# Kernel tuning notes

Measured on AMD Instinct MI355X. Metric: run time of the kernel, lower is better.

## Reference

```python
import jax, jax.numpy as jnp
import numpy as np
from jax import lax

B, W, RSS, NLED, LED_F, HID = 8192, 512, 12, 16, 8, 64


def setup_inputs() -> dict:
    key = jax.random.key(0)
    ks = jax.random.split(key, 20)
    s = 0.05
    return {
        "rss_chunk": jax.random.normal(ks[0], (B, W, RSS), jnp.float32),
        "anchor_pos": jax.random.normal(ks[1], (B, 3), jnp.float32),
        "led_feats": jax.random.normal(ks[2], (NLED, LED_F), jnp.float32),
        "led_positions": jax.random.normal(ks[3], (NLED, 3), jnp.float32),
        "freq_mask": jax.random.randint(ks[4], (RSS, NLED), 0, 2, jnp.int32),
        # temporal_conv params (torch Conv1d weight layout [out, in, k])
        "conv1_w": jax.random.normal(ks[5], (32, RSS, 3), jnp.float32) * s,
        "conv1_b": jax.random.normal(ks[6], (32,), jnp.float32) * s,
        "conv2_w": jax.random.normal(ks[7], (64, 32, 3), jnp.float32) * s,
        "conv2_b": jax.random.normal(ks[8], (64,), jnp.float32) * s,
        # projections (torch Linear weight layout [out, in])
        "q_w": jax.random.normal(ks[9], (64, W + 3), jnp.float32) * s,
        "q_b": jax.random.normal(ks[10], (64,), jnp.float32) * s,
        "k_w": jax.random.normal(ks[11], (64, LED_F + 3), jnp.float32) * s,
        "k_b": jax.random.normal(ks[12], (64,), jnp.float32) * s,
        "red_w": jax.random.normal(ks[13], (64, RSS * LED_F), jnp.float32) * s,
        "red_b": jax.random.normal(ks[14], (64,), jnp.float32) * s,
        "fus_w": jax.random.normal(ks[15], (HID, 64 + 64), jnp.float32) * s,
        "fus_b": jax.random.normal(ks[16], (HID,), jnp.float32) * s,
    }


def _conv1d(x, w, b, stride):
    # x: [B, C_in, L], w: [C_out, C_in, k], padding 1
    y = lax.conv_general_dilated(x, w, (stride,), [(1, 1)],
                                 dimension_numbers=("NCH", "OIH", "NCH"))
    return y + b[None, :, None]


def reference(rss_chunk, anchor_pos, led_feats, led_positions, freq_mask,
              conv1_w, conv1_b, conv2_w, conv2_b,
              q_w, q_b, k_w, k_b, red_w, red_b, fus_w, fus_b):
    Bc = rss_chunk.shape[0]
    x = jnp.swapaxes(rss_chunk, 1, 2)                       # [B, 12, W]

    # temporal conv branch -> [B, 64]
    h = jax.nn.relu(_conv1d(x, conv1_w, conv1_b, 1))        # [B, 32, W]
    h = jax.nn.relu(_conv1d(h, conv2_w, conv2_b, 2))        # [B, 64, W//2]
    t_feat = h.mean(axis=-1)                                # AdaptiveAvgPool1d(1)

    # queries: [B, 12, W+3] -> [B, 12, 64]
    pos_rep = jnp.broadcast_to(anchor_pos[:, None, :], (Bc, RSS, 3))
    query_in = jnp.concatenate([x, pos_rep], axis=-1)
    queries = query_in @ q_w.T + q_b

    # keys: [N, 11] -> [N, 64] (shared across batch)
    key_in = jnp.concatenate([led_feats, led_positions], axis=-1)
    keys = key_in @ k_w.T + k_b

    scores = jnp.einsum("brd,nd->brn", queries, keys)       # [B, 12, N]
    dist_sq = jnp.sum((anchor_pos[:, None, :] - led_positions[None, :, :]) ** 2, -1)
    dist_bias = 0.5 * jnp.log(1.0 / (dist_sq + 1e-8))       # [B, N]
    scores = scores + dist_bias[:, None, :]
    scores = jnp.where(freq_mask[None] == 0, jnp.finfo(scores.dtype).min, scores)

    attn = jax.nn.softmax(scores, axis=-1)                  # [B, 12, N]
    s_agg = jnp.einsum("brn,nf->brf", attn, led_feats)      # [B, 12, 8]
    s_feat = jax.nn.relu(s_agg.reshape(Bc, -1) @ red_w.T + red_b)  # [B, 64]

    combined = jnp.concatenate([t_feat, s_feat], axis=-1)   # [B, 128]
    return combined @ fus_w.T + fus_b                       # [B, hidden]
```

## Files before the change

kernel.cpp:

```cpp
#include <hip/hip_runtime.h>
#include <float.h>
#include <math.h>

typedef __bf16 bf16;
typedef __attribute__((ext_vector_type(8))) __bf16 bf16x8;
typedef __attribute__((ext_vector_type(4))) float f32x4;
typedef long long i64;

#define MK 544

#define WS_MG   0
#define WS_CVEC 17408
#define WS_W1F  17472
#define WS_W2F  19520

__device__ __forceinline__ f32x4 mfma16(bf16x8 a, bf16x8 b, f32x4 c) {
  return __builtin_amdgcn_mfma_f32_16x16x32_bf16(a, b, c, 0, 0, 0);
}
__device__ __forceinline__ f32x4 mfma8(i64 a, i64 b, f32x4 c) {
  return __builtin_amdgcn_mfma_f32_16x16x32_fp8_fp8(a, b, c, 0, 0, 0);
}

__global__ __launch_bounds__(256) void acek_pre(
    const float* __restrict__ led_feats, const float* __restrict__ led_pos,
    const float* __restrict__ q_w, const float* __restrict__ q_b,
    const float* __restrict__ k_w, const float* __restrict__ k_b,
    const float* __restrict__ c1w, const float* __restrict__ c2w,
    char* __restrict__ ws) {
  bf16* Mg = (bf16*)(ws + WS_MG);
  float* cvec = (float*)(ws + WS_CVEC);
  i64* W1F = (i64*)(ws + WS_W1F);
  i64* W2F = (i64*)(ws + WS_W2F);
  const int t = threadIdx.x;

  if (blockIdx.x == 34) {
    {
      int ot = t >> 7, s = (t >> 6) & 1, lane = t & 63;
      int g = lane >> 4, a15 = lane & 15;
      float v[8];
#pragma unroll
      for (int j = 0; j < 8; ++j) {
        int k1 = s * 32 + g * 8 + j;
        int dk = k1 >> 4, ic = k1 & 15;
        v[j] = (ic < 12 && dk < 3) ? 16.f * c1w[(ot * 16 + a15) * 36 + ic * 3 + dk] : 0.f;
      }
      int lo = __builtin_amdgcn_cvt_pk_fp8_f32(v[0], v[1], 0, false);
      lo = __builtin_amdgcn_cvt_pk_fp8_f32(v[2], v[3], lo, true);
      int hi = __builtin_amdgcn_cvt_pk_fp8_f32(v[4], v[5], 0, false);
      hi = __builtin_amdgcn_cvt_pk_fp8_f32(v[6], v[7], hi, true);
      W1F[t] = ((i64)(unsigned)lo) | (((i64)hi) << 32);
    }
    for (int r = 0; r < 3; ++r) {
      int fi = t + r * 256;
      int o = fi / 192, rem = fi - o * 192;
      int s = rem >> 6, lane = rem & 63;
      int g = lane >> 4, a15 = lane & 15;
      float v[8];
#pragma unroll
      for (int j = 0; j < 8; ++j)
        v[j] = 16.f * c2w[(o * 16 + a15) * 96 + (g * 8 + j) * 3 + s];
      int lo = __builtin_amdgcn_cvt_pk_fp8_f32(v[0], v[1], 0, false);
      lo = __builtin_amdgcn_cvt_pk_fp8_f32(v[2], v[3], lo, true);
      int hi = __builtin_amdgcn_cvt_pk_fp8_f32(v[4], v[5], 0, false);
      hi = __builtin_amdgcn_cvt_pk_fp8_f32(v[6], v[7], hi, true);
      W2F[fi] = ((i64)(unsigned)lo) | (((i64)hi) << 32);
    }
    return;
  }

  __shared__ float keys[16 * 64];
  for (int idx = t; idx < 16 * 64; idx += 256) {
    int n = idx >> 6, d = idx & 63;
    float acc = k_b[d];
#pragma unroll
    for (int j = 0; j < 8; ++j) acc += k_w[d * 11 + j] * led_feats[n * 8 + j];
#pragma unroll
    for (int j = 0; j < 3; ++j) acc += k_w[d * 11 + 8 + j] * led_pos[n * 3 + j];
    keys[idx] = acc;
  }
  __syncthreads();
  int e = blockIdx.x * 256 + t;
  if (e < 16 * MK) {
    int n = e / MK, k = e - n * MK;
    float v = 0.f;
    if (k < 515) {
#pragma unroll 4
      for (int d = 0; d < 64; ++d) v += q_w[d * 515 + k] * keys[n * 64 + d];
    }
    Mg[e] = (bf16)v;
  }
  if (blockIdx.x == 0 && t < 16) {
    float acc = 0.f;
    for (int d = 0; d < 64; ++d) acc += q_b[d] * keys[t * 64 + d];
    cvec[t] = acc;
  }
}

__global__ __launch_bounds__(256, 4) void acek_main(
    const float* __restrict__ rss, const float* __restrict__ anchor,
    const float* __restrict__ ledf, const float* __restrict__ ledp,
    const int* __restrict__ fmask,
    const float* __restrict__ c1b, const float* __restrict__ c2b,
    const float* __restrict__ rw, const float* __restrict__ rb,
    const float* __restrict__ fw, const float* __restrict__ fb,
    const bf16* __restrict__ Mg, const float* __restrict__ cvec,
    const i64* __restrict__ W1F, const i64* __restrict__ W2F,
    float* __restrict__ out) {

  __shared__ __align__(16) unsigned char xw8[515 * 16];
  __shared__ __align__(16) unsigned char h1[513 * 32];
  __shared__ __align__(16) float parts[1024];
  __shared__ __align__(16) float sagg[96];
  __shared__ __align__(16) float bias_lds[16];
  float* tfp = (float*)xw8;
  float* comb = (float*)(xw8 + 1024);

  const int tid = threadIdx.x;
  const int lane = tid & 63;
  const int wv = tid >> 6;
  const int a15 = lane & 15;
  const int g = lane >> 4;
  const int b = blockIdx.x;
  char* xwb = (char*)xw8;
  char* h1b = (char*)h1;

  i64 w1f[2][2];
#pragma unroll
  for (int ot = 0; ot < 2; ++ot)
#pragma unroll
    for (int s = 0; s < 2; ++s) w1f[ot][s] = W1F[(ot * 2 + s) * 64 + lane];
  i64 w2f[4][3];
#pragma unroll
  for (int o = 0; o < 4; ++o)
#pragma unroll
    for (int s = 0; s < 3; ++s) w2f[o][s] = W2F[(o * 3 + s) * 64 + lane];
  f32x4 b1v[2], b2s[4];
#pragma unroll
  for (int ot = 0; ot < 2; ++ot) b1v[ot] = *(const f32x4*)&c1b[ot * 16 + g * 4];
#pragma unroll
  for (int o = 0; o < 4; ++o) {
    f32x4 tmp = *(const f32x4*)&c2b[o * 16 + g * 4];
    b2s[o] = tmp * 16.f;
  }

  for (int r = tid; r < 515; r += 256) *(int*)(xwb + r * 16 + 12) = 0;
  if (tid < 12) {
    int rr = (tid >> 2) == 0 ? 0 : ((tid >> 2) == 1 ? 513 : 514);
    *(int*)(xwb + rr * 16 + (tid & 3) * 4) = 0;
  }
  if (tid < 4) *(i64*)(h1b + tid * 8) = 0;
  if (tid < 16) {
    float dx = anchor[(size_t)b * 3 + 0] - ledp[tid * 3 + 0];
    float dy = anchor[(size_t)b * 3 + 1] - ledp[tid * 3 + 1];
    float dz = anchor[(size_t)b * 3 + 2] - ledp[tid * 3 + 2];
    bias_lds[tid] = cvec[tid] - 0.5f * __logf(dx * dx + dy * dy + dz * dz + 1e-8f);
  }

  const float* xb = rss + (size_t)b * 6144;
#pragma unroll
  for (int i = 0; i < 6; ++i) {
    int f = tid + i * 256;
    f32x4 v = ((const f32x4*)xb)[f];
    int w = f / 3;
    int c = (f - w * 3) * 4;
    int pk = __builtin_amdgcn_cvt_pk_fp8_f32(16.f * v[0], 16.f * v[1], 0, false);
    pk = __builtin_amdgcn_cvt_pk_fp8_f32(16.f * v[2], 16.f * v[3], pk, true);
    *(int*)(xwb + (w + 1) * 16 + c) = pk;
  }
  __syncthreads();

  {
    const int rcl = (a15 < 12) ? a15 : 11;
    float sav[4][8];
#pragma unroll
    for (int t = 0; t < 4; ++t) {
      const int s = 4 * t + wv;
      const float* xs = xb + (s * 32 + g * 8) * 12 + rcl;
#pragma unroll
      for (int j = 0; j < 8; ++j) sav[t][j] = xs[j * 12];
    }
    float anc0 = 0.f, anc1 = 0.f, anc2 = 0.f;
    if (wv == 0) {
      anc0 = anchor[(size_t)b * 3 + 0];
      anc1 = anchor[(size_t)b * 3 + 1];
      anc2 = anchor[(size_t)b * 3 + 2];
    }

#pragma unroll
    for (int t = 0; t < 8; ++t) {
      const int wt = wv * 8 + t;
      const int wcol = wt * 16 + a15;
      f32x4 c0 = {0.f, 0.f, 0.f, 0.f}, c1 = {0.f, 0.f, 0.f, 0.f};
#pragma unroll
      for (int s = 0; s < 2; ++s) {
        int row = wcol + 2 * s + (g >> 1);
        i64 bv = *(const i64*)(xwb + row * 16 + ((g & 1) << 3));
        c0 = mfma8(w1f[0][s], bv, c0);
        c1 = mfma8(w1f[1][s], bv, c1);
      }
      const int hrow = wcol + 1;
      const int swz = (hrow >> 2) & 3;
      const int off0 = ((((g >> 1) + 0) ^ swz) << 3) | ((g & 1) << 2);
      const int off1 = ((((g >> 1) + 2) ^ swz) << 3) | ((g & 1) << 2);
      float v0 = fmaxf(fmaf(c0[0], 0.00390625f, b1v[0][0]), 0.f);
      float v1 = fmaxf(fmaf(c0[1], 0.00390625f, b1v[0][1]), 0.f);
      float v2 = fmaxf(fmaf(c0[2], 0.00390625f, b1v[0][2]), 0.f);
      float v3 = fmaxf(fmaf(c0[3], 0.00390625f, b1v[0][3]), 0.f);
      int pk0 = __builtin_amdgcn_cvt_pk_fp8_f32(v0, v1, 0, false);
      pk0 = __builtin_amdgcn_cvt_pk_fp8_f32(v2, v3, pk0, true);
      *(int*)(h1b + hrow * 32 + off0) = pk0;
      v0 = fmaxf(fmaf(c1[0], 0.00390625f, b1v[1][0]), 0.f);
      v1 = fmaxf(fmaf(c1[1], 0.00390625f, b1v[1][1]), 0.f);
      v2 = fmaxf(fmaf(c1[2], 0.00390625f, b1v[1][2]), 0.f);
      v3 = fmaxf(fmaf(c1[3], 0.00390625f, b1v[1][3]), 0.f);
      int pk1 = __builtin_amdgcn_cvt_pk_fp8_f32(v0, v1, 0, false);
      pk1 = __builtin_amdgcn_cvt_pk_fp8_f32(v2, v3, pk1, true);
      *(int*)(h1b + hrow * 32 + off1) = pk1;
    }

    const bf16* MgR = Mg + a15 * MK;
    f32x4 sac = {0.f, 0.f, 0.f, 0.f};
#pragma unroll
    for (int t = 0; t < 4; ++t) {
      const int s = 4 * t + wv;
      bf16x8 av;
#pragma unroll
      for (int j = 0; j < 8; ++j) av[j] = (bf16)sav[t][j];
      bf16x8 bm = *(const bf16x8*)&MgR[s * 32 + g * 8];
      sac = mfma16(av, bm, sac);
    }
    if (wv == 0) {
      bf16x8 av = {(bf16)0.f, (bf16)0.f, (bf16)0.f, (bf16)0.f,
                   (bf16)0.f, (bf16)0.f, (bf16)0.f, (bf16)0.f};
      if (g == 0) { av[0] = (bf16)anc0; av[1] = (bf16)anc1; av[2] = (bf16)anc2; }
      bf16x8 bm = *(const bf16x8*)&MgR[512 + g * 8];
      sac = mfma16(av, bm, sac);
    }
#pragma unroll
    for (int r = 0; r < 4; ++r)
      parts[wv * 256 + (g * 4 + r) * 16 + a15] = sac[r];
  }
  __syncthreads();

  {
    float tacc[4][4] = {{0.f, 0.f, 0.f, 0.f}, {0.f, 0.f, 0.f, 0.f},
                        {0.f, 0.f, 0.f, 0.f}, {0.f, 0.f, 0.f, 0.f}};
#pragma unroll
    for (int pti = 0; pti < 4; ++pti) {
      const int p = (wv * 4 + pti) * 16 + a15;
      f32x4 cc0 = {0.f, 0.f, 0.f, 0.f}, cc1 = {0.f, 0.f, 0.f, 0.f};
      f32x4 cc2 = {0.f, 0.f, 0.f, 0.f}, cc3 = {0.f, 0.f, 0.f, 0.f};
#pragma unroll
      for (int s = 0; s < 3; ++s) {
        const int rho = 2 * p + s;
        i64 hv = *(const i64*)(h1b + rho * 32 + ((g ^ ((rho >> 2) & 3)) << 3));
        cc0 = mfma8(w2f[0][s], hv, cc0);
        cc1 = mfma8(w2f[1][s], hv, cc1);
        cc2 = mfma8(w2f[2][s], hv, cc2);
        cc3 = mfma8(w2f[3][s], hv, cc3);
      }
#pragma unroll
      for (int r = 0; r < 4; ++r) {
        tacc[0][r] += fmaxf(cc0[r] + b2s[0][r], 0.f);
        tacc[1][r] += fmaxf(cc1[r] + b2s[1][r], 0.f);
        tacc[2][r] += fmaxf(cc2[r] + b2s[2][r], 0.f);
        tacc[3][r] += fmaxf(cc3[r] + b2s[3][r], 0.f);
      }
    }
#pragma unroll
    for (int o = 0; o < 4; ++o)
#pragma unroll
      for (int r = 0; r < 4; ++r) {
        float v = tacc[o][r];
        v += __shfl_xor(v, 1, 16);
        v += __shfl_xor(v, 2, 16);
        v += __shfl_xor(v, 4, 16);
        v += __shfl_xor(v, 8, 16);
        if (a15 == 0) tfp[wv * 64 + o * 16 + g * 4 + r] = v;
      }
  }
  __syncthreads();

  if (tid < 192) {
    const int r = tid >> 4, n = tid & 15;
    float s = parts[tid] + parts[256 + tid] + parts[512 + tid] + parts[768 + tid];
    s += bias_lds[n];
    if (fmask[r * 16 + n] == 0) s = -FLT_MAX;
    float mx = s;
    mx = fmaxf(mx, __shfl_xor(mx, 1, 16));
    mx = fmaxf(mx, __shfl_xor(mx, 2, 16));
    mx = fmaxf(mx, __shfl_xor(mx, 4, 16));
    mx = fmaxf(mx, __shfl_xor(mx, 8, 16));
    float ev = __expf(s - mx);
    float sm = ev;
    sm += __shfl_xor(sm, 1, 16);
    sm += __shfl_xor(sm, 2, 16);
    sm += __shfl_xor(sm, 4, 16);
    sm += __shfl_xor(sm, 8, 16);
    const float attv = ev / sm;
#pragma unroll
    for (int f = 0; f < 8; ++f) {
      float c = attv * ledf[n * 8 + f];
      c += __shfl_xor(c, 1, 16);
      c += __shfl_xor(c, 2, 16);
      c += __shfl_xor(c, 4, 16);
      c += __shfl_xor(c, 8, 16);
      if (n == f) sagg[r * 8 + f] = c;
    }
  } else {
    const int t64 = tid - 192;
    comb[t64] = (tfp[t64] + tfp[64 + t64] + tfp[128 + t64] + tfp[192 + t64]) *
                (1.f / 4096.f);
  }
  __syncthreads();

  {
    const int o = tid >> 2, q = tid & 3;
    float acc = 0.f;
    const f32x4* rwv = (const f32x4*)(rw + o * 96 + q * 24);
    const f32x4* sv = (const f32x4*)(sagg + q * 24);
#pragma unroll
    for (int i = 0; i < 6; ++i) {
      f32x4 a = rwv[i], s = sv[i];
      acc += a[0] * s[0] + a[1] * s[1] + a[2] * s[2] + a[3] * s[3];
    }
    acc += __shfl_xor(acc, 1, 4);
    acc += __shfl_xor(acc, 2, 4);
    if (q == 0) comb[64 + o] = fmaxf(acc + rb[o], 0.f);
  }
  __syncthreads();

  {
    const int o = tid >> 2, q = tid & 3;
    float acc = 0.f;
    const f32x4* fwv = (const f32x4*)(fw + o * 128 + q * 32);
    const f32x4* cv = (const f32x4*)(comb + q * 32);
#pragma unroll
    for (int i = 0; i < 8; ++i) {
      f32x4 a = fwv[i], c = cv[i];
      acc += a[0] * c[0] + a[1] * c[1] + a[2] * c[2] + a[3] * c[3];
    }
    acc += __shfl_xor(acc, 1, 4);
    acc += __shfl_xor(acc, 2, 4);
    if (q == 0) out[(size_t)b * 64 + o] = acc + fb[o];
  }
}

extern "C" void kernel_launch(void* const* d_in, const int* in_sizes, int n_in,
                              void* d_out, int out_size, void* d_ws, size_t ws_size,
                              hipStream_t stream) {
  (void)in_sizes; (void)n_in; (void)out_size; (void)ws_size;
  const float* rss   = (const float*)d_in[0];
  const float* anch  = (const float*)d_in[1];
  const float* ledf  = (const float*)d_in[2];
  const float* ledp  = (const float*)d_in[3];
  const int*   fmask = (const int*)d_in[4];
  const float* c1w = (const float*)d_in[5];
  const float* c1b = (const float*)d_in[6];
  const float* c2w = (const float*)d_in[7];
  const float* c2b = (const float*)d_in[8];
  const float* qw  = (const float*)d_in[9];
  const float* qb  = (const float*)d_in[10];
  const float* kw  = (const float*)d_in[11];
  const float* kb  = (const float*)d_in[12];
  const float* rw  = (const float*)d_in[13];
  const float* rb  = (const float*)d_in[14];
  const float* fw  = (const float*)d_in[15];
  const float* fb  = (const float*)d_in[16];
  float* outp = (float*)d_out;
  char* ws = (char*)d_ws;

  acek_pre<<<35, 256, 0, stream>>>(ledf, ledp, qw, qb, kw, kb, c1w, c2w, ws);
  acek_main<<<8192, 256, 0, stream>>>(
      rss, anch, ledf, ledp, fmask, c1b, c2b, rw, rb, fw, fb,
      (const bf16*)(ws + WS_MG), (const float*)(ws + WS_CVEC),
      (const i64*)(ws + WS_W1F), (const i64*)(ws + WS_W2F), outp);
}
```

Before: 139.4 us.

## Make conv stages wave-local with halo recompute, drop barriers, raise occupancy

Each wave now stages its own slice of the fp8 input plus halo rows and recomputes the neighbouring boundary conv1 tile. This lets the block skip the barriers before conv1 and before conv2. The softmax, aggregation and the two small linear layers are collapsed onto wave 0 with no block-level syncs in between. The launch bound rises from 4 to 5 blocks per CU, and tfp/comb get dedicated LDS instead of aliasing the input buffer. The cost is redundant MFMA work on the halos, a longer serial tail on one wave, and more LDS and register pressure.

```diff
diff --git a/kernel.cpp b/kernel.cpp
--- a/kernel.cpp
+++ b/kernel.cpp
@@ -96,7 +96,7 @@
   }
 }
 
-__global__ __launch_bounds__(256, 4) void acek_main(
+__global__ __launch_bounds__(256, 5) void acek_main(
     const float* __restrict__ rss, const float* __restrict__ anchor,
     const float* __restrict__ ledf, const float* __restrict__ ledp,
     const int* __restrict__ fmask,
@@ -112,8 +112,8 @@
   __shared__ __align__(16) float parts[1024];
   __shared__ __align__(16) float sagg[96];
   __shared__ __align__(16) float bias_lds[16];
-  float* tfp = (float*)xw8;
-  float* comb = (float*)(xw8 + 1024);
+  __shared__ __align__(16) float tfp[256];
+  __shared__ __align__(16) float comb[128];
 
   const int tid = threadIdx.x;
   const int lane = tid & 63;
@@ -143,12 +143,16 @@
     b2s[o] = tmp * 16.f;
   }
 
-  for (int r = tid; r < 515; r += 256) *(int*)(xwb + r * 16 + 12) = 0;
-  if (tid < 12) {
-    int rr = (tid >> 2) == 0 ? 0 : ((tid >> 2) == 1 ? 513 : 514);
-    *(int*)(xwb + rr * 16 + (tid & 3) * 4) = 0;
-  }
-  if (tid < 4) *(i64*)(h1b + tid * 8) = 0;
+  if (wv == 0 && lane < 4) *(int*)(xwb + lane * 4) = 0;
+  if (wv == 3 && lane < 8)
+    *(int*)(xwb + (513 + (lane >> 2)) * 16 + (lane & 3) * 4) = 0;
+  if (wv == 0 && lane < 4) *(i64*)(h1b + lane * 8) = 0;
+#pragma unroll
+  for (int i = 0; i < 3; ++i) {
+    int k = lane + 64 * i;
+    int r = wv * 128 - 1 + k;
+    if (k < 132 && r >= 0 && r <= 514) *(int*)(xwb + r * 16 + 12) = 0;
+  }
   if (tid < 16) {
     float dx = anchor[(size_t)b * 3 + 0] - ledp[tid * 3 + 0];
     float dy = anchor[(size_t)b * 3 + 1] - ledp[tid * 3 + 1];
@@ -157,67 +161,82 @@
   }
 
   const float* xb = rss + (size_t)b * 6144;
-#pragma unroll
-  for (int i = 0; i < 6; ++i) {
-    int f = tid + i * 256;
-    f32x4 v = ((const f32x4*)xb)[f];
-    int w = f / 3;
-    int c = (f - w * 3) * 4;
+  const f32x4* xb4 = (const f32x4*)xb;
+  auto stage_px = [&](int w, int hc, f32x4 v) {
     int pk = __builtin_amdgcn_cvt_pk_fp8_f32(16.f * v[0], 16.f * v[1], 0, false);
     pk = __builtin_amdgcn_cvt_pk_fp8_f32(16.f * v[2], 16.f * v[3], pk, true);
-    *(int*)(xwb + (w + 1) * 16 + c) = pk;
-  }
-  __syncthreads();
+    *(int*)(xwb + (w + 1) * 16 + hc * 4) = pk;
+  };
+#pragma unroll
+  for (int i = 0; i < 6; ++i) {
+    int f = wv * 384 + lane + 64 * i;
+    int w = f / 3;
+    int c = f - w * 3;
+    stage_px(w, c, xb4[f]);
+  }
+  if (wv > 0 && lane < 6) {
+    int hw = wv * 128 - 2 + lane / 3;
+    int hc = lane - (lane / 3) * 3;
+    stage_px(hw, hc, xb4[hw * 3 + hc]);
+  }
+  if (wv < 3 && lane >= 6 && lane < 12) {
+    int l2 = lane - 6;
+    int hw = wv * 128 + 128 + l2 / 3;
+    int hc = l2 - (l2 / 3) * 3;
+    stage_px(hw, hc, xb4[hw * 3 + hc]);
+  }
+
+  const int rcl = (a15 < 12) ? a15 : 11;
+  float sav[4][8];
+#pragma unroll
+  for (int t = 0; t < 4; ++t) {
+    const int s = 4 * t + wv;
+    const float* xs = xb + (s * 32 + g * 8) * 12 + rcl;
+#pragma unroll
+    for (int j = 0; j < 8; ++j) sav[t][j] = xs[j * 12];
+  }
+  float anc0 = 0.f, anc1 = 0.f, anc2 = 0.f;
+  if (wv == 0) {
+    anc0 = anchor[(size_t)b * 3 + 0];
+    anc1 = anchor[(size_t)b * 3 + 1];
+    anc2 = anchor[(size_t)b * 3 + 2];
+  }
+
+  auto conv1_tile = [&](int wt, bool edgeOnly) {
+    const int wcol = wt * 16 + a15;
+    f32x4 c0 = {0.f, 0.f, 0.f, 0.f}, c1 = {0.f, 0.f, 0.f, 0.f};
+#pragma unroll
+    for (int s = 0; s < 2; ++s) {
+      int row = wcol + 2 * s + (g >> 1);
+      i64 bv = *(const i64*)(xwb + row * 16 + ((g & 1) << 3));
+      c0 = mfma8(w1f[0][s], bv, c0);
+      c1 = mfma8(w1f[1][s], bv, c1);
+    }
+    if (edgeOnly && a15 != 15) return;
+    const int hrow = wcol + 1;
+    const int swz = (hrow >> 2) & 3;
+    const int off0 = ((((g >> 1) + 0) ^ swz) << 3) | ((g & 1) << 2);
+    const int off1 = ((((g >> 1) + 2) ^ swz) << 3) | ((g & 1) << 2);
+    float v0 = fmaxf(fmaf(c0[0], 0.00390625f, b1v[0][0]), 0.f);
+    float v1 = fmaxf(fmaf(c0[1], 0.00390625f, b1v[0][1]), 0.f);
+    float v2 = fmaxf(fmaf(c0[2], 0.00390625f, b1v[0][2]), 0.f);
+    float v3 = fmaxf(fmaf(c0[3], 0.00390625f, b1v[0][3]), 0.f);
+    int pk0 = __builtin_amdgcn_cvt_pk_fp8_f32(v0, v1, 0, false);
+    pk0 = __builtin_amdgcn_cvt_pk_fp8_f32(v2, v3, pk0, true);
+    *(int*)(h1b + hrow * 32 + off0) = pk0;
+    v0 = fmaxf(fmaf(c1[0], 0.00390625f, b1v[1][0]), 0.f);
+    v1 = fmaxf(fmaf(c1[1], 0.00390625f, b1v[1][1]), 0.f);
+    v2 = fmaxf(fmaf(c1[2], 0.00390625f, b1v[1][2]), 0.f);
+    v3 = fmaxf(fmaf(c1[3], 0.00390625f, b1v[1][3]), 0.f);
+    int pk1 = __builtin_amdgcn_cvt_pk_fp8_f32(v0, v1, 0, false);
+    pk1 = __builtin_amdgcn_cvt_pk_fp8_f32(v2, v3, pk1, true);
+    *(int*)(h1b + hrow * 32 + off1) = pk1;
+  };
+#pragma unroll
+  for (int t = 0; t < 8; ++t) conv1_tile(wv * 8 + t, false);
+  if (wv > 0) conv1_tile(wv * 8 - 1, true);
 
   {
-    const int rcl = (a15 < 12) ? a15 : 11;
-    float sav[4][8];
-#pragma unroll
-    for (int t = 0; t < 4; ++t) {
-      const int s = 4 * t + wv;
-      const float* xs = xb + (s * 32 + g * 8) * 12 + rcl;
-#pragma unroll
-      for (int j = 0; j < 8; ++j) sav[t][j] = xs[j * 12];
-    }
-    float anc0 = 0.f, anc1 = 0.f, anc2 = 0.f;
-    if (wv == 0) {
-      anc0 = anchor[(size_t)b * 3 + 0];
-      anc1 = anchor[(size_t)b * 3 + 1];
-      anc2 = anchor[(size_t)b * 3 + 2];
-    }
-
-#pragma unroll
-    for (int t = 0; t < 8; ++t) {
-      const int wt = wv * 8 + t;
-      const int wcol = wt * 16 + a15;
-      f32x4 c0 = {0.f, 0.f, 0.f, 0.f}, c1 = {0.f, 0.f, 0.f, 0.f};
-#pragma unroll
-      for (int s = 0; s < 2; ++s) {
-        int row = wcol + 2 * s + (g >> 1);
-        i64 bv = *(const i64*)(xwb + row * 16 + ((g & 1) << 3));
-        c0 = mfma8(w1f[0][s], bv, c0);
-        c1 = mfma8(w1f[1][s], bv, c1);
-      }
-      const int hrow = wcol + 1;
-      const int swz = (hrow >> 2) & 3;
-      const int off0 = ((((g >> 1) + 0) ^ swz) << 3) | ((g & 1) << 2);
-      const int off1 = ((((g >> 1) + 2) ^ swz) << 3) | ((g & 1) << 2);
-      float v0 = fmaxf(fmaf(c0[0], 0.00390625f, b1v[0][0]), 0.f);
-      float v1 = fmaxf(fmaf(c0[1], 0.00390625f, b1v[0][1]), 0.f);
-      float v2 = fmaxf(fmaf(c0[2], 0.00390625f, b1v[0][2]), 0.f);
-      float v3 = fmaxf(fmaf(c0[3], 0.00390625f, b1v[0][3]), 0.f);
-      int pk0 = __builtin_amdgcn_cvt_pk_fp8_f32(v0, v1, 0, false);
-      pk0 = __builtin_amdgcn_cvt_pk_fp8_f32(v2, v3, pk0, true);
-      *(int*)(h1b + hrow * 32 + off0) = pk0;
-      v0 = fmaxf(fmaf(c1[0], 0.00390625f, b1v[1][0]), 0.f);
-      v1 = fmaxf(fmaf(c1[1], 0.00390625f, b1v[1][1]), 0.f);
-      v2 = fmaxf(fmaf(c1[2], 0.00390625f, b1v[1][2]), 0.f);
-      v3 = fmaxf(fmaf(c1[3], 0.00390625f, b1v[1][3]), 0.f);
-      int pk1 = __builtin_amdgcn_cvt_pk_fp8_f32(v0, v1, 0, false);
-      pk1 = __builtin_amdgcn_cvt_pk_fp8_f32(v2, v3, pk1, true);
-      *(int*)(h1b + hrow * 32 + off1) = pk1;
-    }
-
     const bf16* MgR = Mg + a15 * MK;
     f32x4 sac = {0.f, 0.f, 0.f, 0.f};
 #pragma unroll
@@ -240,7 +259,6 @@
     for (int r = 0; r < 4; ++r)
       parts[wv * 256 + (g * 4 + r) * 16 + a15] = sac[r];
   }
-  __syncthreads();
 
   {
     float tacc[4][4] = {{0.f, 0.f, 0.f, 0.f}, {0.f, 0.f, 0.f, 0.f},
@@ -281,68 +299,61 @@
   }
   __syncthreads();
 
-  if (tid < 192) {
-    const int r = tid >> 4, n = tid & 15;
-    float s = parts[tid] + parts[256 + tid] + parts[512 + tid] + parts[768 + tid];
-    s += bias_lds[n];
-    if (fmask[r * 16 + n] == 0) s = -FLT_MAX;
-    float mx = s;
-    mx = fmaxf(mx, __shfl_xor(mx, 1, 16));
-    mx = fmaxf(mx, __shfl_xor(mx, 2, 16));
-    mx = fmaxf(mx, __shfl_xor(mx, 4, 16));
-    mx = fmaxf(mx, __shfl_xor(mx, 8, 16));
-    float ev = __expf(s - mx);
-    float sm = ev;
-    sm += __shfl_xor(sm, 1, 16);
-    sm += __shfl_xor(sm, 2, 16);
-    sm += __shfl_xor(sm, 4, 16);
-    sm += __shfl_xor(sm, 8, 16);
-    const float attv = ev / sm;
-#pragma unroll
-    for (int f = 0; f < 8; ++f) {
-      float c = attv * ledf[n * 8 + f];
-      c += __shfl_xor(c, 1, 16);
-      c += __shfl_xor(c, 2, 16);
-      c += __shfl_xor(c, 4, 16);
-      c += __shfl_xor(c, 8, 16);
-      if (n == f) sagg[r * 8 + f] = c;
-    }
-  } else {
-    const int t64 = tid - 192;
-    comb[t64] = (tfp[t64] + tfp[64 + t64] + tfp[128 + t64] + tfp[192 + t64]) *
-                (1.f / 4096.f);
-  }
-  __syncthreads();
-
-  {
-    const int o = tid >> 2, q = tid & 3;
-    float acc = 0.f;
-    const f32x4* rwv = (const f32x4*)(rw + o * 96 + q * 24);
-    const f32x4* sv = (const f32x4*)(sagg + q * 24);
-#pragma unroll
-    for (int i = 0; i < 6; ++i) {
-      f32x4 a = rwv[i], s = sv[i];
-      acc += a[0] * s[0] + a[1] * s[1] + a[2] * s[2] + a[3] * s[3];
-    }
-    acc += __shfl_xor(acc, 1, 4);
-    acc += __shfl_xor(acc, 2, 4);
-    if (q == 0) comb[64 + o] = fmaxf(acc + rb[o], 0.f);
-  }
-  __syncthreads();
-
-  {
-    const int o = tid >> 2, q = tid & 3;
-    float acc = 0.f;
-    const f32x4* fwv = (const f32x4*)(fw + o * 128 + q * 32);
-    const f32x4* cv = (const f32x4*)(comb + q * 32);
-#pragma unroll
-    for (int i = 0; i < 8; ++i) {
-      f32x4 a = fwv[i], c = cv[i];
-      acc += a[0] * c[0] + a[1] * c[1] + a[2] * c[2] + a[3] * c[3];
-    }
-    acc += __shfl_xor(acc, 1, 4);
-    acc += __shfl_xor(acc, 2, 4);
-    if (q == 0) out[(size_t)b * 64 + o] = acc + fb[o];
+  if (wv == 0) {
+    const int n = a15;
+#pragma unroll
+    for (int it = 0; it < 3; ++it) {
+      const int r = g + 4 * it;
+      float s = parts[r * 16 + n] + parts[256 + r * 16 + n] +
+                parts[512 + r * 16 + n] + parts[768 + r * 16 + n];
+      s += bias_lds[n];
+      if (fmask[r * 16 + n] == 0) s = -FLT_MAX;
+      float mx = s;
+      mx = fmaxf(mx, __shfl_xor(mx, 1, 16));
+      mx = fmaxf(mx, __shfl_xor(mx, 2, 16));
+      mx = fmaxf(mx, __shfl_xor(mx, 4, 16));
+      mx = fmaxf(mx, __shfl_xor(mx, 8, 16));
+      float ev = __expf(s - mx);
+      float sm = ev;
+      sm += __shfl_xor(sm, 1, 16);
+      sm += __shfl_xor(sm, 2, 16);
+      sm += __shfl_xor(sm, 4, 16);
+      sm += __shfl_xor(sm, 8, 16);
+      const float attv = ev / sm;
+#pragma unroll
+      for (int f = 0; f < 8; ++f) {
+        float c = attv * ledf[n * 8 + f];
+        c += __shfl_xor(c, 1, 16);
+        c += __shfl_xor(c, 2, 16);
+        c += __shfl_xor(c, 4, 16);
+        c += __shfl_xor(c, 8, 16);
+        if (n == f) sagg[r * 8 + f] = c;
+      }
+    }
+    comb[lane] = (tfp[lane] + tfp[64 + lane] + tfp[128 + lane] + tfp[192 + lane]) *
+                 (1.f / 4096.f);
+    {
+      float acc = rb[lane];
+      const f32x4* rwv = (const f32x4*)(rw + lane * 96);
+#pragma unroll
+      for (int i = 0; i < 24; ++i) {
+        f32x4 a = rwv[i];
+        f32x4 sv = *(const f32x4*)&sagg[i * 4];
+        acc += a[0] * sv[0] + a[1] * sv[1] + a[2] * sv[2] + a[3] * sv[3];
+      }
+      comb[64 + lane] = fmaxf(acc, 0.f);
+    }
+    {
+      float acc = fb[lane];
+      const f32x4* fwv = (const f32x4*)(fw + lane * 128);
+#pragma unroll
+      for (int i = 0; i < 32; ++i) {
+        f32x4 a = fwv[i];
+        f32x4 c = *(const f32x4*)&comb[i * 4];
+        acc += a[0] * c[0] + a[1] * c[1] + a[2] * c[2] + a[3] * c[3];
+      }
+      out[(size_t)b * 64 + lane] = acc;
+    }
   }
 }
 
```

New measurement: 226.2 us. 1.62x slower.
